# Kernel optimization log

Hardware: AMD Instinct MI355X
Metric: run time of the kernel (lower is better)

Reference implementation:

```python
import jax, jax.numpy as jnp
import numpy as np

B, I, H = 16384, 1024, 1024

def setup_inputs() -> dict:
    key = jax.random.key(0)
    ks = jax.random.split(key, 6)
    s_i = 1.0 / np.sqrt(I)
    s_h = 1.0 / np.sqrt(H)
    return {
        "incoming": jax.random.normal(ks[0], (B, I), dtype=jnp.float32),
        "old_h": jax.random.normal(ks[1], (B, H), dtype=jnp.float32),
        "old_c": jax.random.normal(ks[2], (B, H), dtype=jnp.float32),
        # 4 gates stacked: order [i, f, g, o] matching the torch ModuleList indices 0..3
        "Wi": jax.random.uniform(ks[3], (4, H, I), minval=-s_i, maxval=s_i, dtype=jnp.float32),
        "bi": jax.random.uniform(ks[4], (4, H), minval=-s_i, maxval=s_i, dtype=jnp.float32),
        "Wh": jax.random.uniform(ks[5], (4, H, H), minval=-s_h, maxval=s_h, dtype=jnp.float32),
    }

def reference(incoming, old_h, old_c, Wi, bi, Wh):
    # two batched GEMMs producing all 4 gate pre-activations: [4, B, H]
    gates = (jnp.einsum('bi,ghi->gbh', incoming, Wi)
             + jnp.einsum('bh,gkh->gbk', old_h, Wh)
             + bi[:, None, :])
    i = jax.nn.sigmoid(gates[0])
    f = jax.nn.sigmoid(gates[1])
    g = jnp.tanh(gates[2])
    o = jax.nn.sigmoid(gates[3])
    new_c = f * old_c + i * g
    new_h = o * jnp.tanh(new_c)
    return (new_h, (new_h, new_c))
```

## Files before the change

### kernel.cpp

```cpp
#include <hip/hip_runtime.h>
#include <hip/hip_bf16.h>
#include <math.h>

#define B_SZ 16384
#define H_SZ 1024
#define K_SZ 2048
#define OUT_PLANE ((size_t)B_SZ * H_SZ)

#define BM 128
#define BH 32
#define BK 64

typedef __bf16 bf16;
typedef __attribute__((ext_vector_type(8))) __bf16 bf16x8;
typedef __attribute__((ext_vector_type(4))) float floatx4;

__device__ __forceinline__ void gload_lds16(const bf16* g, bf16* l) {
    __builtin_amdgcn_global_load_lds(
        (const __attribute__((address_space(1))) void*)g,
        (__attribute__((address_space(3))) void*)l, 16, 0, 0);
}

__device__ __forceinline__ float sigmoidf_fast(float x) {
    return 1.f / (1.f + __expf(-x));
}
__device__ __forceinline__ float tanhf_fast(float x) {
    return 2.f / (1.f + __expf(-2.f * x)) - 1.f;
}

__global__ void cvt_all(const float* __restrict__ inc, const float* __restrict__ oh,
                        const float* __restrict__ Wi, const float* __restrict__ Wh,
                        bf16* __restrict__ X, bf16* __restrict__ W) {
    const size_t nX = (size_t)B_SZ * K_SZ;
    size_t t  = (size_t)blockIdx.x * blockDim.x + threadIdx.x;
    size_t e0 = t * 8;
    const float* src;
    bf16* dst;
    if (e0 < nX) {
        size_t b = e0 >> 11;
        int    k = (int)(e0 & 2047);
        src = (k < 1024) ? (inc + b * 1024 + k) : (oh + b * 1024 + (k - 1024));
        dst = X + e0;
    } else {
        size_t e = e0 - nX;
        size_t n = e >> 11;
        int    k = (int)(e & 2047);
        src = (k < 1024) ? (Wi + n * 1024 + k) : (Wh + n * 1024 + (k - 1024));
        dst = W + e;
    }
    floatx4 f0 = *(const floatx4*)src;
    floatx4 f1 = *(const floatx4*)(src + 4);
    bf16x8 o;
    o[0]=(bf16)f0[0]; o[1]=(bf16)f0[1]; o[2]=(bf16)f0[2]; o[3]=(bf16)f0[3];
    o[4]=(bf16)f1[0]; o[5]=(bf16)f1[1]; o[6]=(bf16)f1[2]; o[7]=(bf16)f1[3];
    *(bf16x8*)dst = o;
}

__global__ __launch_bounds__(256, 4) void lstm_gemm(
    const bf16* __restrict__ X, const bf16* __restrict__ W,
    const float* __restrict__ bi, const float* __restrict__ oldc,
    float* __restrict__ out) {
    __shared__ bf16 As[BM * BK];
    __shared__ bf16 Bs[128 * BK];

    const int tid  = threadIdx.x;
    const int lane = tid & 63;
    const int wv   = tid >> 6;
    const int h0   = blockIdx.x * BH;
    const int brow0 = blockIdx.y * BM;

    floatx4 acc[4][2][2];
    #pragma unroll
    for (int g = 0; g < 4; ++g)
        #pragma unroll
        for (int n = 0; n < 2; ++n)
            #pragma unroll
            for (int m = 0; m < 2; ++m) {
                floatx4 z = {0.f, 0.f, 0.f, 0.f};
                acc[g][n][m] = z;
            }

    const int lrow = lane >> 3;
    const int lcol = (((lane & 7) ^ lrow) * 8);

    const bf16* xg = X + (size_t)(brow0 + wv * 8 + lrow) * K_SZ + lcol;

    for (int kt = 0; kt < K_SZ; kt += BK) {
        #pragma unroll
        for (int r = 0; r < 4; ++r) {
            gload_lds16(xg + (size_t)(r * 32) * K_SZ + kt,
                        As + (r * 32 + wv * 8) * BK);
        }
        #pragma unroll
        for (int r = 0; r < 4; ++r) {
            int rb   = r * 32 + wv * 8 + lrow;
            int wrow = ((rb >> 5) << 10) + h0 + (rb & 31);
            gload_lds16(W + (size_t)wrow * K_SZ + kt + lcol,
                        Bs + (r * 32 + wv * 8) * BK);
        }
        __syncthreads();

        #pragma unroll
        for (int kk = 0; kk < BK; kk += 32) {
            const int q    = lane >> 4;
            const int cidx = (kk >> 3) + q;
            const int arow0 = wv * 32 + (lane & 15);
            const int arow1 = arow0 + 16;
            bf16x8 a0 = *(const bf16x8*)(
                As + (size_t)arow0 * BK + ((cidx ^ (arow0 & 7)) * 8));
            bf16x8 a1 = *(const bf16x8*)(
                As + (size_t)arow1 * BK + ((cidx ^ (arow1 & 7)) * 8));
            #pragma unroll
            for (int g = 0; g < 4; ++g) {
                #pragma unroll
                for (int n = 0; n < 2; ++n) {
                    const int brow = g * 32 + n * 16 + (lane & 15);
                    bf16x8 bfr = *(const bf16x8*)(
                        Bs + (size_t)brow * BK + ((cidx ^ (brow & 7)) * 8));
                    acc[g][n][0] = __builtin_amdgcn_mfma_f32_16x16x32_bf16(
                        a0, bfr, acc[g][n][0], 0, 0, 0);
                    acc[g][n][1] = __builtin_amdgcn_mfma_f32_16x16x32_bf16(
                        a1, bfr, acc[g][n][1], 0, 0, 0);
                }
            }
        }
        __syncthreads();
    }

    float* outh  = out;
    float* outh2 = out + OUT_PLANE;
    float* outc  = out + 2 * OUT_PLANE;
    #pragma unroll
    for (int n = 0; n < 2; ++n) {
        const int h  = h0 + n * 16 + (lane & 15);
        const float b_i = bi[h];
        const float b_f = bi[H_SZ + h];
        const float b_g = bi[2 * H_SZ + h];
        const float b_o = bi[3 * H_SZ + h];
        #pragma unroll
        for (int m = 0; m < 2; ++m) {
            const int brow = brow0 + wv * 32 + m * 16 + ((lane >> 4) << 2);
            #pragma unroll
            for (int r = 0; r < 4; ++r) {
                const size_t idx = (size_t)(brow + r) * H_SZ + h;
                float gi = acc[0][n][m][r] + b_i;
                float gf = acc[1][n][m][r] + b_f;
                float gg = acc[2][n][m][r] + b_g;
                float go = acc[3][n][m][r] + b_o;
                float iv = sigmoidf_fast(gi);
                float fv = sigmoidf_fast(gf);
                float gv = tanhf_fast(gg);
                float ov = sigmoidf_fast(go);
                float c  = fv * oldc[idx] + iv * gv;
                float hv = ov * tanhf_fast(c);
                outh[idx]  = hv;
                outh2[idx] = hv;
                outc[idx]  = c;
            }
        }
    }
}

__global__ void lstm_fallback(const float* __restrict__ X, const float* __restrict__ Ho,
                              const float* __restrict__ Co, const float* __restrict__ Wi,
                              const float* __restrict__ bi, const float* __restrict__ Wh,
                              float* __restrict__ out) {
    int b = blockIdx.x;
    __shared__ float xs[1024], hs[1024];
    for (int k = threadIdx.x; k < 1024; k += blockDim.x) {
        xs[k] = X[(size_t)b * 1024 + k];
        hs[k] = Ho[(size_t)b * 1024 + k];
    }
    __syncthreads();
    for (int h = threadIdx.x; h < 1024; h += blockDim.x) {
        float g[4];
        for (int gg = 0; gg < 4; ++gg) {
            const float* wi = Wi + ((size_t)gg * 1024 + h) * 1024;
            const float* wh = Wh + ((size_t)gg * 1024 + h) * 1024;
            float acc = bi[gg * 1024 + h];
        for (int k = 0; k < 1024; ++k) acc += xs[k] * wi[k] + hs[k] * wh[k];
            g[gg] = acc;
        }
        float iv = sigmoidf_fast(g[0]);
        float fv = sigmoidf_fast(g[1]);
        float gv = tanhf_fast(g[2]);
        float ov = sigmoidf_fast(g[3]);
        float c  = fv * Co[(size_t)b * 1024 + h] + iv * gv;
        float hv = ov * tanhf_fast(c);
        size_t idx = (size_t)b * 1024 + h;
        out[idx] = hv;
        out[OUT_PLANE + idx] = hv;
        out[2 * OUT_PLANE + idx] = c;
    }
}

extern "C" void kernel_launch(void* const* d_in, const int* in_sizes, int n_in,
                              void* d_out, int out_size, void* d_ws, size_t ws_size,
                              hipStream_t stream) {
    const float* incoming = (const float*)d_in[0];
    const float* old_h    = (const float*)d_in[1];
    const float* old_c    = (const float*)d_in[2];
    const float* Wi       = (const float*)d_in[3];
    const float* bi       = (const float*)d_in[4];
    const float* Wh       = (const float*)d_in[5];
    float* out = (float*)d_out;

    const size_t nX = (size_t)B_SZ * K_SZ;
    const size_t nW = (size_t)4 * H_SZ * K_SZ;
    if (ws_size < (nX + nW) * sizeof(bf16)) {
        lstm_fallback<<<B_SZ, 256, 0, stream>>>(incoming, old_h, old_c, Wi, bi, Wh, out);
        return;
    }
    bf16* X = (bf16*)d_ws;
    bf16* W = X + nX;

    const int cvt_blocks = (int)((nX + nW) / 8 / 256);
    cvt_all<<<cvt_blocks, 256, 0, stream>>>(incoming, old_h, Wi, Wh, X, W);

    dim3 grid(H_SZ / BH, B_SZ / BM);
    lstm_gemm<<<grid, 256, 0, stream>>>(X, W, bi, old_c, out);
}
```

Baseline: 607.1 us.

## Enlarge GEMM tiles and double-buffer LDS with interleaved async loads

The fused LSTM GEMM moves to 512-thread blocks with a 256x(4x64) output tile. It double-buffers the A and B LDS tiles and splits each K-step into four quarter-phases, so global-to-LDS loads for the next step are issued while MFMAs run on the current one. Blocks are swizzled so neighbouring blocks share row and column tiles in L2, and MFMA sections raise wave priority. The larger tile raises arithmetic intensity and hides load latency, at the cost of more registers, occupancy capped at 2 blocks per CU, and hand-placed waitcnt and barrier logic that must be exactly right.

```diff
diff --git a/kernel.cpp b/kernel.cpp
--- a/kernel.cpp
+++ b/kernel.cpp
@@ -7,9 +7,10 @@
 #define K_SZ 2048
 #define OUT_PLANE ((size_t)B_SZ * H_SZ)
 
-#define BM 128
-#define BH 32
+#define BM 256
+#define BNH 64
 #define BK 64
+#define NKT (K_SZ / BK)
 
 typedef __bf16 bf16;
 typedef __attribute__((ext_vector_type(8))) __bf16 bf16x8;
@@ -20,6 +21,9 @@
         (const __attribute__((address_space(1))) void*)g,
         (__attribute__((address_space(3))) void*)l, 16, 0, 0);
 }
+
+__device__ __forceinline__ void bar() { asm volatile("s_barrier" ::: "memory"); }
+#define WAIT_VM(n) asm volatile("s_waitcnt vmcnt(" #n ")" ::: "memory")
 
 __device__ __forceinline__ float sigmoidf_fast(float x) {
     return 1.f / (1.f + __expf(-x));
@@ -56,107 +60,157 @@
     *(bf16x8*)dst = o;
 }
 
-__global__ __launch_bounds__(256, 4) void lstm_gemm(
+__device__ __forceinline__ void stageA(const bf16* xg, bf16* dst, int h, int ktn, int wv) {
+    gload_lds16(xg + (size_t)(h * 64) * K_SZ + ktn, dst + (h * 64 + wv * 8) * BK);
+    gload_lds16(xg + (size_t)(128 + h * 64) * K_SZ + ktn, dst + (128 + h * 64 + wv * 8) * BK);
+}
+__device__ __forceinline__ void stageB(const bf16* wg, bf16* dst, int hb, int ktn, int wv) {
+    gload_lds16(wg + (size_t)((2 * hb) * 1024) * K_SZ + ktn, dst + ((2 * hb) * 64 + wv * 8) * BK);
+    gload_lds16(wg + (size_t)((2 * hb + 1) * 1024) * K_SZ + ktn, dst + ((2 * hb + 1) * 64 + wv * 8) * BK);
+}
+
+__global__ __launch_bounds__(512, 2) void lstm_gemm(
     const bf16* __restrict__ X, const bf16* __restrict__ W,
     const float* __restrict__ bi, const float* __restrict__ oldc,
     float* __restrict__ out) {
-    __shared__ bf16 As[BM * BK];
-    __shared__ bf16 Bs[128 * BK];
+    __shared__ bf16 As[2][BM * BK];
+    __shared__ bf16 Bs[2][BM * BK];
 
     const int tid  = threadIdx.x;
     const int lane = tid & 63;
     const int wv   = tid >> 6;
-    const int h0   = blockIdx.x * BH;
-    const int brow0 = blockIdx.y * BM;
-
-    floatx4 acc[4][2][2];
+    const int wm   = wv >> 2;
+    const int wn   = wv & 3;
+    const int q    = lane >> 4;
+    const int r16  = lane & 15;
+    const int lrow = lane >> 3;
+    const int gch  = (lane & 7) ^ lrow;
+
+    const int id = blockIdx.y * 16 + blockIdx.x;
+    const int sw = (id & 7) * 128 + (id >> 3);
+    const int h0    = (sw & 15) * BNH;
+    const int brow0 = (sw >> 4) * BM;
+
+    const bf16* xg = X + (size_t)(brow0 + wv * 8 + lrow) * K_SZ + gch * 8;
+    const bf16* wg = W + (size_t)(h0 + wv * 8 + lrow) * K_SZ + gch * 8;
+
+    floatx4 acc[8][4];
     #pragma unroll
-    for (int g = 0; g < 4; ++g)
+    for (int mg = 0; mg < 8; ++mg)
         #pragma unroll
-        for (int n = 0; n < 2; ++n)
-            #pragma unroll
-            for (int m = 0; m < 2; ++m) {
-                floatx4 z = {0.f, 0.f, 0.f, 0.f};
-                acc[g][n][m] = z;
-            }
-
-    const int lrow = lane >> 3;
-    const int lcol = (((lane & 7) ^ lrow) * 8);
-
-    const bf16* xg = X + (size_t)(brow0 + wv * 8 + lrow) * K_SZ + lcol;
-
-    for (int kt = 0; kt < K_SZ; kt += BK) {
-        #pragma unroll
-        for (int r = 0; r < 4; ++r) {
-            gload_lds16(xg + (size_t)(r * 32) * K_SZ + kt,
-                        As + (r * 32 + wv * 8) * BK);
+        for (int g = 0; g < 4; ++g) {
+            floatx4 z = {0.f, 0.f, 0.f, 0.f};
+            acc[mg][g] = z;
         }
-        #pragma unroll
-        for (int r = 0; r < 4; ++r) {
-            int rb   = r * 32 + wv * 8 + lrow;
-            int wrow = ((rb >> 5) << 10) + h0 + (rb & 31);
-            gload_lds16(W + (size_t)wrow * K_SZ + kt + lcol,
-                        Bs + (r * 32 + wv * 8) * BK);
-        }
-        __syncthreads();
-
-        #pragma unroll
-        for (int kk = 0; kk < BK; kk += 32) {
-            const int q    = lane >> 4;
-            const int cidx = (kk >> 3) + q;
-            const int arow0 = wv * 32 + (lane & 15);
-            const int arow1 = arow0 + 16;
-            bf16x8 a0 = *(const bf16x8*)(
-                As + (size_t)arow0 * BK + ((cidx ^ (arow0 & 7)) * 8));
-            bf16x8 a1 = *(const bf16x8*)(
-                As + (size_t)arow1 * BK + ((cidx ^ (arow1 & 7)) * 8));
-            #pragma unroll
-            for (int g = 0; g < 4; ++g) {
-                #pragma unroll
-                for (int n = 0; n < 2; ++n) {
-                    const int brow = g * 32 + n * 16 + (lane & 15);
-                    bf16x8 bfr = *(const bf16x8*)(
-                        Bs + (size_t)brow * BK + ((cidx ^ (brow & 7)) * 8));
-                    acc[g][n][0] = __builtin_amdgcn_mfma_f32_16x16x32_bf16(
-                        a0, bfr, acc[g][n][0], 0, 0, 0);
-                    acc[g][n][1] = __builtin_amdgcn_mfma_f32_16x16x32_bf16(
-                        a1, bfr, acc[g][n][1], 0, 0, 0);
-                }
-            }
-        }
-        __syncthreads();
-    }
+
+    bf16x8 Af[4][2];
+    bf16x8 Bf[4][2];
+
+#define LDA(mh) do { \
+    _Pragma("unroll") for (int m = 0; m < 4; ++m) { \
+        const int row = wm * 128 + (mh) * 64 + m * 16 + r16; \
+        const bf16* base = rA + (size_t)row * BK; \
+        _Pragma("unroll") for (int ks = 0; ks < 2; ++ks) \
+            Af[m][ks] = *(const bf16x8*)(base + (((ks * 4 + q) ^ (row & 7)) * 8)); \
+    } } while (0)
+
+#define LDB(nh) do { \
+    _Pragma("unroll") for (int gg = 0; gg < 2; ++gg) { \
+        const int row = ((nh) * 2 + gg) * 64 + wn * 16 + r16; \
+        const bf16* base = rB + (size_t)row * BK; \
+        _Pragma("unroll") for (int ks = 0; ks < 2; ++ks) \
+            Bf[(nh) * 2 + gg][ks] = *(const bf16x8*)(base + (((ks * 4 + q) ^ (row & 7)) * 8)); \
+    } } while (0)
+
+#define MMA(mh, nh) do { \
+    __builtin_amdgcn_s_setprio(1); \
+    _Pragma("unroll") for (int m = 0; m < 4; ++m) \
+    _Pragma("unroll") for (int gg = 0; gg < 2; ++gg) \
+    _Pragma("unroll") for (int ks = 0; ks < 2; ++ks) \
+        acc[(mh) * 4 + m][(nh) * 2 + gg] = __builtin_amdgcn_mfma_f32_16x16x32_bf16( \
+            Af[m][ks], Bf[(nh) * 2 + gg][ks], acc[(mh) * 4 + m][(nh) * 2 + gg], 0, 0, 0); \
+    __builtin_amdgcn_s_setprio(0); \
+} while (0)
+
+    const bf16* rA = As[0];
+    const bf16* rB = Bs[0];
+    bf16* wAp = As[1];
+    bf16* wBp = Bs[1];
+
+    stageA(xg, As[0], 0, 0, wv);
+    stageB(wg, Bs[0], 0, 0, wv);
+    stageB(wg, Bs[0], 1, 0, wv);
+    stageA(xg, As[0], 1, 0, wv);
+
+    for (int t = 0; t < NKT - 1; ++t) {
+        const int ktn = (t + 1) * BK;
+        WAIT_VM(4); bar();
+        LDA(0); LDB(0);
+        stageA(xg, wAp, 0, ktn, wv);
+        MMA(0, 0);
+        bar();
+        WAIT_VM(4); bar();
+        LDB(1);
+        stageB(wg, wBp, 0, ktn, wv);
+        MMA(0, 1);
+        bar();
+        WAIT_VM(4); bar();
+        LDA(1);
+        stageB(wg, wBp, 1, ktn, wv);
+        MMA(1, 1);
+        bar();
+        stageA(xg, wAp, 1, ktn, wv);
+        MMA(1, 0);
+        bar();
+        const bf16* tA = rA; rA = wAp; wAp = (bf16*)tA;
+        const bf16* tB = rB; rB = wBp; wBp = (bf16*)tB;
+    }
+
+    WAIT_VM(4); bar();
+    LDA(0); LDB(0);
+    MMA(0, 0);
+    bar();
+    WAIT_VM(2); bar();
+    LDB(1);
+    MMA(0, 1);
+    bar();
+    WAIT_VM(0); bar();
+    LDA(1);
+    MMA(1, 1);
+    bar();
+    MMA(1, 0);
+
+#undef LDA
+#undef LDB
+#undef MMA
 
     float* outh  = out;
     float* outh2 = out + OUT_PLANE;
     float* outc  = out + 2 * OUT_PLANE;
+    const int h = h0 + wn * 16 + r16;
+    const float b_i = bi[h];
+    const float b_f = bi[H_SZ + h];
+    const float b_g = bi[2 * H_SZ + h];
+    const float b_o = bi[3 * H_SZ + h];
     #pragma unroll
-    for (int n = 0; n < 2; ++n) {
-        const int h  = h0 + n * 16 + (lane & 15);
-        const float b_i = bi[h];
-        const float b_f = bi[H_SZ + h];
-        const float b_g = bi[2 * H_SZ + h];
-        const float b_o = bi[3 * H_SZ + h];
+    for (int mg = 0; mg < 8; ++mg) {
+        const int brow = brow0 + wm * 128 + mg * 16 + q * 4;
         #pragma unroll
-        for (int m = 0; m < 2; ++m) {
-            const int brow = brow0 + wv * 32 + m * 16 + ((lane >> 4) << 2);
-            #pragma unroll
-            for (int r = 0; r < 4; ++r) {
-                const size_t idx = (size_t)(brow + r) * H_SZ + h;
-                float gi = acc[0][n][m][r] + b_i;
-                float gf = acc[1][n][m][r] + b_f;
-                float gg = acc[2][n][m][r] + b_g;
-                float go = acc[3][n][m][r] + b_o;
-                float iv = sigmoidf_fast(gi);
-                float fv = sigmoidf_fast(gf);
-                float gv = tanhf_fast(gg);
-                float ov = sigmoidf_fast(go);
-                float c  = fv * oldc[idx] + iv * gv;
-                float hv = ov * tanhf_fast(c);
-                outh[idx]  = hv;
-                outh2[idx] = hv;
-                outc[idx]  = c;
-            }
+        for (int rr = 0; rr < 4; ++rr) {
+            const size_t idx = (size_t)(brow + rr) * H_SZ + h;
+            float gi = acc[mg][0][rr] + b_i;
+            float gf = acc[mg][1][rr] + b_f;
+            float gv_ = acc[mg][2][rr] + b_g;
+            float go = acc[mg][3][rr] + b_o;
+            float iv = sigmoidf_fast(gi);
+            float fv = sigmoidf_fast(gf);
+            float gv = tanhf_fast(gv_);
+            float ov = sigmoidf_fast(go);
+            float c  = fv * oldc[idx] + iv * gv;
+            float hv = ov * tanhf_fast(c);
+            outh[idx]  = hv;
+            outh2[idx] = hv;
+            outc[idx]  = c;
         }
     }
 }
@@ -178,7 +232,7 @@
             const float* wi = Wi + ((size_t)gg * 1024 + h) * 1024;
             const float* wh = Wh + ((size_t)gg * 1024 + h) * 1024;
             float acc = bi[gg * 1024 + h];
-        for (int k = 0; k < 1024; ++k) acc += xs[k] * wi[k] + hs[k] * wh[k];
+            for (int k = 0; k < 1024; ++k) acc += xs[k] * wi[k] + hs[k] * wh[k];
             g[gg] = acc;
         }
         float iv = sigmoidf_fast(g[0]);
@@ -217,6 +271,6 @@
     const int cvt_blocks = (int)((nX + nW) / 8 / 256);
     cvt_all<<<cvt_blocks, 256, 0, stream>>>(incoming, old_h, Wi, Wh, X, W);
 
-    dim3 grid(H_SZ / BH, B_SZ / BM);
-    lstm_gemm<<<grid, 256, 0, stream>>>(X, W, bi, old_c, out);
-}
+    dim3 grid(H_SZ / BNH, B_SZ / BM);
+    lstm_gemm<<<grid, 512, 0, stream>>>(X, W, bi, old_c, out);
+}
```

After: 600.4 us. About the same (-1.1%).
